# Kernel optimization log

Hardware: AMD Instinct MI355X
Metric: run time of the kernel (lower is better)

The kernel has to match this reference:

```python
import jax, jax.numpy as jnp
import numpy as np
import math

D_MODEL = 1024
N_HEADS = 16
D_HEAD = D_MODEL // N_HEADS
B, T = 2, 2048


def setup_inputs() -> dict:
    key = jax.random.key(0)
    ks = jax.random.split(key, 5)
    x = jax.random.normal(ks[0], (B, T, D_MODEL), dtype=jnp.float32)
    W_qkv = jax.random.normal(ks[1], (D_MODEL, 3 * D_MODEL), dtype=jnp.float32) * 0.02
    b_qkv = jnp.zeros((3 * D_MODEL,), dtype=jnp.float32)
    W_g = jax.random.normal(ks[2], (N_HEADS, D_HEAD, D_HEAD), dtype=jnp.float32) * 0.02
    W_out = jax.random.normal(ks[3], (D_MODEL, D_MODEL), dtype=jnp.float32) * 0.02
    b_out = jnp.zeros((D_MODEL,), dtype=jnp.float32)
    return {"x": x, "W_qkv": W_qkv, "b_qkv": b_qkv, "W_g": W_g, "W_out": W_out, "b_out": b_out}


def reference(x, W_qkv, b_qkv, W_g, W_out, b_out):
    b, t, d = x.shape
    h, dh = N_HEADS, D_HEAD
    qkv = x @ W_qkv + b_qkv                         # (B,T,3D)
    q, k, v = jnp.split(qkv, 3, axis=-1)
    # (B,T,D) -> (B,H,T,dh)
    q = q.reshape(b, t, h, dh).transpose(0, 2, 1, 3)
    k = k.reshape(b, t, h, dh).transpose(0, 2, 1, 3)
    v = v.reshape(b, t, h, dh).transpose(0, 2, 1, 3)
    scale = 1.0 / math.sqrt(dh)
    scores = jnp.einsum('bhtd,bhsd->bhts', q, k) * scale   # (B,H,T,T)
    causal = jnp.tril(jnp.ones((t, t), dtype=bool))
    scores = jnp.where(causal, scores, jnp.float32(-jnp.inf))
    attn = jax.nn.softmax(scores, axis=-1)
    # query-conditioned bilinear value gate (applied at each position)
    g = jax.nn.sigmoid(jnp.einsum('bhtd,hde->bhte', q, W_g))  # (B,H,T,dh)
    v = g * v
    out = jnp.einsum('bhts,bhsd->bhtd', attn, v)             # (B,H,T,dh)
    out = out.transpose(0, 2, 1, 3).reshape(b, t, d)
    return out @ W_out + b_out
```

## Files before the change

kernel.cpp:

```cpp
#include <hip/hip_runtime.h>
#include <hip/hip_bf16.h>

typedef unsigned short ushortT;
typedef __bf16 bf16x8 __attribute__((ext_vector_type(8)));
typedef float f32x4 __attribute__((ext_vector_type(4)));

#define T_SEQ 2048
#define DH 64
#define NH 16
#define DM 1024
#define TD 3072
#define BATCH 2
#define LOG2E 1.44269504f

#define BARRIER()   asm volatile("s_barrier" ::: "memory")
#define VMCNT(n)    asm volatile("s_waitcnt vmcnt(" #n ")" ::: "memory")

__device__ inline ushortT f2bf(float f){
    union { float f; unsigned int u; } a; a.f = f;
    unsigned int r = a.u + 0x7fffu + ((a.u >> 16) & 1u);
    return (ushortT)(r >> 16);
}
__device__ inline float bf2f(ushortT u){
    union { float f; unsigned int u; } a; a.u = ((unsigned int)u) << 16;
    return a.f;
}

__device__ inline void gload_lds16(const void* g, void* l){
    __builtin_amdgcn_global_load_lds((const __attribute__((address_space(1))) void*)g,
                                     (__attribute__((address_space(3))) void*)l, 16, 0, 0);
}

__global__ __launch_bounds__(256) void prep_kernel(const float* __restrict__ x,
                                                   ushortT* __restrict__ xbf,
                                                   const float* __restrict__ Wqkv,
                                                   ushortT* __restrict__ wqkvT,
                                                   const float* __restrict__ Wout,
                                                   ushortT* __restrict__ woutT,
                                                   const float* __restrict__ Wg,
                                                   ushortT* __restrict__ wgT){
    __shared__ float tile[64][65];
    int blk = blockIdx.x, tid = threadIdx.x;
    if (blk < 4096){
        int i = (blk * 256 + tid) * 4;
        float4 v = *(const float4*)&x[i];
        xbf[i+0] = f2bf(v.x); xbf[i+1] = f2bf(v.y);
        xbf[i+2] = f2bf(v.z); xbf[i+3] = f2bf(v.w);
        return;
    }
    int c = tid & 63, r4 = tid >> 6;
    if (blk >= 5120){
        int h = blk - 5120;
#pragma unroll
        for (int i = 0; i < 16; i++){
            int d = r4 + i*4;
            tile[d][c] = Wg[h*4096 + d*64 + c];
        }
        __syncthreads();
#pragma unroll
        for (int i = 0; i < 16; i++){
            int e = r4 + i*4;
            wgT[h*4096 + e*64 + c] = f2bf(tile[c][e]);
        }
        return;
    }
    const float* in; ushortT* out; int K, N, n0, k0;
    if (blk < 4864){
        int t = blk - 4096; in = Wqkv; out = wqkvT; K = 1024; N = 3072;
        n0 = (t % 48) * 64; k0 = (t / 48) * 64;
    } else {
        int t = blk - 4864; in = Wout; out = woutT; K = 1024; N = 1024;
        n0 = (t & 15) * 64; k0 = (t >> 4) * 64;
    }
#pragma unroll
    for (int i = 0; i < 16; i++){
        int k = r4 + i * 4;
        tile[k][c] = in[(size_t)(k0 + k) * N + n0 + c];
    }
    __syncthreads();
#pragma unroll
    for (int i = 0; i < 16; i++){
        int n = r4 + i * 4;
        out[(size_t)(n0 + n) * K + k0 + c] = f2bf(tile[c][n]);
    }
}

__global__ __launch_bounds__(256) void gemm_bf16_kernel(const ushortT* __restrict__ A,
                                                        const ushortT* __restrict__ BT,
                                                        const float* __restrict__ bias,
                                                        ushortT* __restrict__ C,
                                                        int M, int N, int K){
    __shared__ __align__(16) ushortT As[2][128*32];
    __shared__ __align__(16) ushortT Bs[2][128*32];
    int tid = threadIdx.x;
    int m0 = blockIdx.x * 128;
    int n0 = blockIdx.y * 128;
    int wid = tid >> 6, lane = tid & 63;
    int l15 = lane & 15, g = lane >> 4;
    int wr = wid >> 1, wc = wid & 1;

    f32x4 acc[4][4];
#pragma unroll
    for (int i = 0; i < 4; i++)
#pragma unroll
        for (int j = 0; j < 4; j++) acc[i][j] = (f32x4){0.f,0.f,0.f,0.f};

    int srow = wid * 32 + (lane >> 2);
    int sch  = lane & 3;

#define GSTAGE(buf, k0)                                                                  \
    {                                                                                    \
        _Pragma("unroll")                                                                \
        for (int i_ = 0; i_ < 2; i_++){                                                  \
            int row_ = srow + i_ * 16;                                                   \
            const ushortT* asrc_ = A  + (size_t)(m0 + row_) * K + (k0) + sch * 8;        \
            const ushortT* bsrc_ = BT + (size_t)(n0 + row_) * K + (k0) + sch * 8;        \
            gload_lds16(asrc_, (char*)As[buf] + (wid*2 + i_) * 1024);                    \
            gload_lds16(bsrc_, (char*)Bs[buf] + (wid*2 + i_) * 1024);                    \
        }                                                                                \
    }

    GSTAGE(0, 0);

    int nk = K >> 5;
    for (int kt = 0; kt < nk; kt++){
        int buf = kt & 1;
        BARRIER();
        if (kt + 1 < nk){
            GSTAGE(buf ^ 1, (kt + 1) * 32);
            VMCNT(4);
        } else {
            VMCNT(0);
        }
        BARRIER();

        bf16x8 af[4], bfr[4];
#pragma unroll
        for (int mi = 0; mi < 4; mi++){
            int r = wr*64 + mi*16 + l15;
            af[mi]  = *(const bf16x8*)(As[buf] + r*32 + g*8);
        }
#pragma unroll
        for (int ni = 0; ni < 4; ni++){
            int r = wc*64 + ni*16 + l15;
            bfr[ni] = *(const bf16x8*)(Bs[buf] + r*32 + g*8);
        }
#pragma unroll
        for (int mi = 0; mi < 4; mi++)
#pragma unroll
            for (int ni = 0; ni < 4; ni++)
                acc[mi][ni] = __builtin_amdgcn_mfma_f32_16x16x32_bf16(af[mi], bfr[ni], acc[mi][ni], 0, 0, 0);
    }
#undef GSTAGE

#pragma unroll
    for (int mi = 0; mi < 4; mi++){
#pragma unroll
        for (int jj = 0; jj < 4; jj++){
            int mm = m0 + wr*64 + mi*16 + 4*g + jj;
#pragma unroll
            for (int ni = 0; ni < 4; ni++){
                int nn = n0 + wc*64 + ni*16 + l15;
                C[(size_t)mm * N + nn] = f2bf(acc[mi][ni][jj] + bias[nn]);
            }
        }
    }
}

__global__ __launch_bounds__(256) void gemm_out_kernel(const ushortT* __restrict__ A,
                                                       const ushortT* __restrict__ BT,
                                                       const float* __restrict__ bias,
                                                       float* __restrict__ C,
                                                       int M, int N, int K){
    __shared__ __align__(16) ushortT As[2][64*32];
    __shared__ __align__(16) ushortT Bs[2][128*32];
    int tid = threadIdx.x;
    int m0 = blockIdx.x * 64;
    int n0 = blockIdx.y * 128;
    int wid = tid >> 6, lane = tid & 63;
    int l15 = lane & 15, g = lane >> 4;
    int wr = wid >> 1, wc = wid & 1;

    f32x4 acc[2][4];
#pragma unroll
    for (int i = 0; i < 2; i++)
#pragma unroll
        for (int j = 0; j < 4; j++) acc[i][j] = (f32x4){0.f,0.f,0.f,0.f};

    int srow = tid >> 2;
    int sch  = tid & 3;

#define GSTAGE(buf, k0)                                                                  \
    {                                                                                    \
        gload_lds16(A + (size_t)(m0 + srow) * K + (k0) + sch * 8,                        \
                    (char*)As[buf] + tid * 16);                                          \
        _Pragma("unroll")                                                                \
        for (int i_ = 0; i_ < 2; i_++){                                                  \
            int row_ = srow + i_ * 64;                                                   \
            gload_lds16(BT + (size_t)(n0 + row_) * K + (k0) + sch * 8,                   \
                        (char*)Bs[buf] + (i_*256 + tid) * 16);                           \
        }                                                                                \
    }

    GSTAGE(0, 0);

    int nk = K >> 5;
    for (int kt = 0; kt < nk; kt++){
        int buf = kt & 1;
        BARRIER();
        if (kt + 1 < nk){
            GSTAGE(buf ^ 1, (kt + 1) * 32);
            VMCNT(3);
        } else {
            VMCNT(0);
        }
        BARRIER();

        bf16x8 af[2], bfr[4];
#pragma unroll
        for (int mi = 0; mi < 2; mi++){
            int r = wr*32 + mi*16 + l15;
            af[mi]  = *(const bf16x8*)(As[buf] + r*32 + g*8);
        }
#pragma unroll
        for (int ni = 0; ni < 4; ni++){
            int r = wc*64 + ni*16 + l15;
            bfr[ni] = *(const bf16x8*)(Bs[buf] + r*32 + g*8);
        }
#pragma unroll
        for (int mi = 0; mi < 2; mi++)
#pragma unroll
            for (int ni = 0; ni < 4; ni++)
                acc[mi][ni] = __builtin_amdgcn_mfma_f32_16x16x32_bf16(af[mi], bfr[ni], acc[mi][ni], 0, 0, 0);
    }
#undef GSTAGE

#pragma unroll
    for (int mi = 0; mi < 2; mi++){
#pragma unroll
        for (int jj = 0; jj < 4; jj++){
            int mm = m0 + wr*32 + mi*16 + 4*g + jj;
#pragma unroll
            for (int ni = 0; ni < 4; ni++){
                int nn = n0 + wc*64 + ni*16 + l15;
                C[(size_t)mm * N + nn] = acc[mi][ni][jj] + bias[nn];
            }
        }
    }
}

__global__ __launch_bounds__(256) void gate_kernel(const ushortT* __restrict__ qkv,
                                                   const ushortT* __restrict__ WgT,
                                                   ushortT* __restrict__ vgT){
    __shared__ __align__(16) ushortT VT[64][72];
    int tblk = blockIdx.x, bh = blockIdx.y;
    int b = bh >> 4, h = bh & 15;
    int tid = threadIdx.x, wid = tid >> 6, lane = tid & 63;
    int l15 = lane & 15, g = lane >> 4;
    int t0 = tblk * 64;
    int tl = wid*16 + l15;

    const ushortT* qrow = qkv + ((size_t)b*T_SEQ + t0 + tl)*TD + h*DH;
    bf16x8 qf0 = *(const bf16x8*)(qrow + 8*g);
    bf16x8 qf1 = *(const bf16x8*)(qrow + 32 + 8*g);

    const ushortT* wbase = WgT + h*4096;
    const ushortT* vrow = qkv + ((size_t)b*T_SEQ + t0 + tl)*TD + 2*DM + h*DH;

#pragma unroll
    for (int ns = 0; ns < 4; ns++){
        int e = ns*16 + l15;
        bf16x8 wf0 = *(const bf16x8*)(wbase + e*64 + 8*g);
        bf16x8 wf1 = *(const bf16x8*)(wbase + e*64 + 32 + 8*g);
        f32x4 z = (f32x4){0.f,0.f,0.f,0.f};
        z = __builtin_amdgcn_mfma_f32_16x16x32_bf16(wf0, qf0, z, 0, 0, 0);
        z = __builtin_amdgcn_mfma_f32_16x16x32_bf16(wf1, qf1, z, 0, 0, 0);
        union { ushortT u[4]; uint2 v; } v4;
        v4.v = *(const uint2*)(vrow + ns*16 + 4*g);
#pragma unroll
        for (int jj = 0; jj < 4; jj++){
            float ex = __builtin_amdgcn_exp2f(-z[jj] * LOG2E);
            float gv = __builtin_amdgcn_rcpf(1.f + ex);
            VT[ns*16 + 4*g + jj][tl] = f2bf(gv * bf2f(v4.u[jj]));
        }
    }
    __syncthreads();
    for (int i = tid; i < 64*8; i += 256){
        int e = i >> 3, c8 = (i & 7) * 8;
        *(uint4*)&vgT[((size_t)bh * DH + e) * T_SEQ + t0 + c8] = *(const uint4*)&VT[e][c8];
    }
}

struct QS {
    bf16x8 qf0, qf1;
    float m_, lsum;
    f32x4 acc[4];
};

__device__ __forceinline__ void proc2(const ushortT* __restrict__ K0,
                                      const ushortT* __restrict__ V0,
                                      const ushortT* __restrict__ K1,
                                      const ushortT* __restrict__ V1,
                                      QS& S, int t0, int t1, int myp,
                                      int wq, int l15, int g){
    int l7 = l15 & 7;
    f32x4 s[8];
    __builtin_amdgcn_s_setprio(1);
#pragma unroll
    for (int ns = 0; ns < 4; ns++){
        int kr = ns*16 + l15;
        bf16x8 kf0 = *(const bf16x8*)(K0 + kr*64 + ((g    ) ^ l7)*8);
        bf16x8 kf1 = *(const bf16x8*)(K0 + kr*64 + ((4 + g) ^ l7)*8);
        f32x4 z = (f32x4){0.f,0.f,0.f,0.f};
        z = __builtin_amdgcn_mfma_f32_16x16x32_bf16(kf0, S.qf0, z, 0, 0, 0);
        z = __builtin_amdgcn_mfma_f32_16x16x32_bf16(kf1, S.qf1, z, 0, 0, 0);
        s[ns] = z;
    }
#pragma unroll
    for (int ns = 0; ns < 4; ns++){
        int kr = ns*16 + l15;
        bf16x8 kf0 = *(const bf16x8*)(K1 + kr*64 + ((g    ) ^ l7)*8);
        bf16x8 kf1 = *(const bf16x8*)(K1 + kr*64 + ((4 + g) ^ l7)*8);
        f32x4 z = (f32x4){0.f,0.f,0.f,0.f};
        z = __builtin_amdgcn_mfma_f32_16x16x32_bf16(kf0, S.qf0, z, 0, 0, 0);
        z = __builtin_amdgcn_mfma_f32_16x16x32_bf16(kf1, S.qf1, z, 0, 0, 0);
        s[4 + ns] = z;
    }
    __builtin_amdgcn_s_setprio(0);

    int qrel = wq*16 + l15;
    bool diag0 = (t0 == myp);
    bool inv1  = (t1 > myp);
    bool diag1 = (t1 == myp);
    if (diag0){
#pragma unroll
        for (int ns = 0; ns < 4; ns++){
            int kb = ((ns & 2) << 4) + 8*g + ((ns & 1) << 2);
#pragma unroll
            for (int jj = 0; jj < 4; jj++)
                if (kb + jj > qrel) s[ns][jj] = -INFINITY;
        }
    }
    if (inv1){
#pragma unroll
        for (int ns = 0; ns < 4; ns++)
#pragma unroll
            for (int jj = 0; jj < 4; jj++) s[4+ns][jj] = -INFINITY;
    } else if (diag1){
#pragma unroll
        for (int ns = 0; ns < 4; ns++){
            int kb = ((ns & 2) << 4) + 8*g + ((ns & 1) << 2);
#pragma unroll
            for (int jj = 0; jj < 4; jj++)
                if (kb + jj > qrel) s[4+ns][jj] = -INFINITY;
        }
    }

    float tmax = -INFINITY;
#pragma unroll
    for (int ns = 0; ns < 8; ns++){
        float a = fmaxf(s[ns][0], s[ns][1]);
        float c = fmaxf(s[ns][2], s[ns][3]);
        tmax = fmaxf(tmax, fmaxf(a, c));
    }
    tmax = fmaxf(tmax, __shfl_xor(tmax, 16, 64));
    tmax = fmaxf(tmax, __shfl_xor(tmax, 32, 64));

    float mnew = fmaxf(S.m_, tmax);
    float mc = mnew * LOG2E;
    float rs = 0.f;
    bf16x8 pa[4];
#pragma unroll
    for (int pr = 0; pr < 4; pr++){
#pragma unroll
        for (int jj = 0; jj < 4; jj++){
            float p0 = __builtin_amdgcn_exp2f(fmaf(s[2*pr  ][jj], LOG2E, -mc));
            float p1 = __builtin_amdgcn_exp2f(fmaf(s[2*pr+1][jj], LOG2E, -mc));
            rs += p0 + p1;
            pa[pr][jj]   = (__bf16)p0;
            pa[pr][4+jj] = (__bf16)p1;
        }
    }
    rs += __shfl_xor(rs, 16, 64);
    rs += __shfl_xor(rs, 32, 64);

    if (!__all(mnew == S.m_)){
        float alpha = __builtin_amdgcn_exp2f(fmaf(S.m_, LOG2E, -mc));
#pragma unroll
        for (int nt = 0; nt < 4; nt++)
#pragma unroll
            for (int jj = 0; jj < 4; jj++) S.acc[nt][jj] *= alpha;
        S.lsum *= alpha;
        S.m_ = mnew;
    }
    S.lsum += rs;

    __builtin_amdgcn_s_setprio(1);
#pragma unroll
    for (int ks = 0; ks < 2; ks++){
#pragma unroll
        for (int nt = 0; nt < 4; nt++){
            bf16x8 vf = *(const bf16x8*)(V0 + (nt*16 + l15)*64 + ((ks*4 + g) ^ l7)*8);
            S.acc[nt] = __builtin_amdgcn_mfma_f32_16x16x32_bf16(vf, pa[ks], S.acc[nt], 0, 0, 0);
        }
    }
    if (!inv1){
#pragma unroll
        for (int ks = 0; ks < 2; ks++){
#pragma unroll
            for (int nt = 0; nt < 4; nt++){
                bf16x8 vf = *(const bf16x8*)(V1 + (nt*16 + l15)*64 + ((ks*4 + g) ^ l7)*8);
                S.acc[nt] = __builtin_amdgcn_mfma_f32_16x16x32_bf16(vf, pa[2+ks], S.acc[nt], 0, 0, 0);
            }
        }
    }
    __builtin_amdgcn_s_setprio(0);
}

__global__ __launch_bounds__(512, 2) void attn_kernel(const ushortT* __restrict__ qkv,
                                                      const ushortT* __restrict__ vgT,
                                                      ushortT* __restrict__ obf){
    __shared__ __align__(16) ushortT Ks[2][2][64*64];
    __shared__ __align__(16) ushortT Vs[2][2][64*64];
    int bh = blockIdx.x, y = blockIdx.y;
    int pairid = (y < 8) ? y : 23 - y;
    int b = bh >> 4, h = bh & 15;
    int tid = threadIdx.x, wid = tid >> 6, lane = tid & 63;
    int l15 = lane & 15, g = lane >> 4;
    int grp = wid >> 2;
    int wq  = wid & 3;

    const ushortT* Kg = qkv + (size_t)b * T_SEQ * TD + DM + h * DH;
    const ushortT* Vg = vgT + (size_t)bh * DH * T_SEQ;

    int pA = pairid, pB = 31 - pairid;
    int myp = grp ? pB : pA;

    int st_row  = tid >> 3;
    int st_c    = (tid & 7) ^ (st_row & 7);
    int st_prow = (st_row & 0x20) | ((st_row & 0x0C) << 1) |
                  ((st_row & 0x10) >> 2) | (st_row & 3);

#define STAGE_ROUND(buf, rr)                                                             \
    {                                                                                    \
        int t0_ = 2*(rr);     if (t0_ > pB) t0_ = pB;                                    \
        int t1_ = 2*(rr) + 1; if (t1_ > pB) t1_ = pB;                                    \
        gload_lds16(Kg + (size_t)(t0_*64 + st_prow) * TD + st_c*8,                       \
                    (char*)Ks[buf][0] + tid*16);                                         \
        gload_lds16(Kg + (size_t)(t1_*64 + st_prow) * TD + st_c*8,                       \
                    (char*)Ks[buf][1] + tid*16);                                         \
        gload_lds16(Vg + (size_t)st_row * T_SEQ + t0_*64 + st_c*8,                       \
                    (char*)Vs[buf][0] + tid*16);                                         \
        gload_lds16(Vg + (size_t)st_row * T_SEQ + t1_*64 + st_c*8,                       \
                    (char*)Vs[buf][1] + tid*16);                                         \
    }

    QS S;
    {
        int qrow = myp*64 + wq*16 + l15;
        const ushortT* qb = qkv + ((size_t)b * T_SEQ + qrow) * TD + h * DH;
        S.qf0 = *(const bf16x8*)(qb + 8*g);
        S.qf1 = *(const bf16x8*)(qb + 32 + 8*g);
#pragma unroll
        for (int j = 0; j < 8; j++){
            S.qf0[j] = (__bf16)((float)S.qf0[j] * 0.125f);
            S.qf1[j] = (__bf16)((float)S.qf1[j] * 0.125f);
        }
        S.m_ = -INFINITY; S.lsum = 0.f;
#pragma unroll
        for (int nt = 0; nt < 4; nt++) S.acc[nt] = (f32x4){0.f,0.f,0.f,0.f};
    }

    int nr = (33 - pairid) >> 1;
    STAGE_ROUND(0, 0);

    for (int r = 0; r < nr; r++){
        int buf = r & 1;
        BARRIER();
        if (r + 1 < nr){
            STAGE_ROUND(buf ^ 1, r + 1);
            VMCNT(4);
        } else {
            VMCNT(0);
        }
        BARRIER();
        int t0 = 2*r;
        if (t0 <= myp)
            proc2(Ks[buf][0], Vs[buf][0], Ks[buf][1], Vs[buf][1],
                  S, t0, t0 + 1, myp, wq, l15, g);
    }
#undef STAGE_ROUND

    float inv = 1.f / S.lsum;
    size_t orow = ((size_t)b * T_SEQ + myp*64 + wq*16 + l15) * DM + h*DH;
#pragma unroll
    for (int nt = 0; nt < 4; nt++){
        union { ushortT u[4]; uint2 v; } pk;
#pragma unroll
        for (int jj = 0; jj < 4; jj++) pk.u[jj] = f2bf(S.acc[nt][jj] * inv);
        *(uint2*)&obf[orow + nt*16 + 4*g] = pk.v;
    }
}

extern "C" void kernel_launch(void* const* d_in, const int* in_sizes, int n_in,
                              void* d_out, int out_size, void* d_ws, size_t ws_size,
                              hipStream_t stream){
    const float* x    = (const float*)d_in[0];
    const float* Wqkv = (const float*)d_in[1];
    const float* bqkv = (const float*)d_in[2];
    const float* Wg   = (const float*)d_in[3];
    const float* Wout = (const float*)d_in[4];
    const float* bout = (const float*)d_in[5];

    char* ws = (char*)d_ws;
    ushortT* xbf   = (ushortT*)(ws);
    ushortT* wqkvT = (ushortT*)(ws + 8388608);
    ushortT* woutT = (ushortT*)(ws + 14680064);
    ushortT* qkvb  = (ushortT*)(ws + 16777216);
    ushortT* vgT   = (ushortT*)(ws + 41943040);
    ushortT* obf   = (ushortT*)(ws + 50331648);
    ushortT* wgT   = (ushortT*)(ws + 58720256);

    prep_kernel<<<5136, 256, 0, stream>>>(x, xbf, Wqkv, wqkvT, Wout, woutT, Wg, wgT);
    gemm_bf16_kernel<<<dim3(32,24), 256, 0, stream>>>(xbf, wqkvT, bqkv, qkvb, 4096, 3072, 1024);
    gate_kernel<<<dim3(32,32), 256, 0, stream>>>(qkvb, wgT, vgT);
    attn_kernel<<<dim3(32,16), 512, 0, stream>>>(qkvb, vgT, obf);
    gemm_out_kernel<<<dim3(64,8), 256, 0, stream>>>(obf, woutT, bout, (float*)d_out, 4096, 1024, 1024);
}
```

Baseline: 110.1 us.

## Switch attention to 32x32x16 MFMA with 32-row query tiles per wave

```diff
diff --git a/kernel.cpp b/kernel.cpp
--- a/kernel.cpp
+++ b/kernel.cpp
@@ -4,6 +4,7 @@
 typedef unsigned short ushortT;
 typedef __bf16 bf16x8 __attribute__((ext_vector_type(8)));
 typedef float f32x4 __attribute__((ext_vector_type(4)));
+typedef float f32x16 __attribute__((ext_vector_type(16)));
 
 #define T_SEQ 2048
 #define DH 64
@@ -291,133 +292,117 @@
     }
 }
 
-struct QS {
-    bf16x8 qf0, qf1;
+struct QS32 {
+    bf16x8 qf[4];
     float m_, lsum;
-    f32x4 acc[4];
+    f32x16 acc[2];
 };
 
-__device__ __forceinline__ void proc2(const ushortT* __restrict__ K0,
-                                      const ushortT* __restrict__ V0,
-                                      const ushortT* __restrict__ K1,
-                                      const ushortT* __restrict__ V1,
-                                      QS& S, int t0, int t1, int myp,
-                                      int wq, int l15, int g){
-    int l7 = l15 & 7;
-    f32x4 s[8];
-    __builtin_amdgcn_s_setprio(1);
-#pragma unroll
-    for (int ns = 0; ns < 4; ns++){
-        int kr = ns*16 + l15;
-        bf16x8 kf0 = *(const bf16x8*)(K0 + kr*64 + ((g    ) ^ l7)*8);
-        bf16x8 kf1 = *(const bf16x8*)(K0 + kr*64 + ((4 + g) ^ l7)*8);
-        f32x4 z = (f32x4){0.f,0.f,0.f,0.f};
-        z = __builtin_amdgcn_mfma_f32_16x16x32_bf16(kf0, S.qf0, z, 0, 0, 0);
-        z = __builtin_amdgcn_mfma_f32_16x16x32_bf16(kf1, S.qf1, z, 0, 0, 0);
-        s[ns] = z;
-    }
-#pragma unroll
-    for (int ns = 0; ns < 4; ns++){
-        int kr = ns*16 + l15;
-        bf16x8 kf0 = *(const bf16x8*)(K1 + kr*64 + ((g    ) ^ l7)*8);
-        bf16x8 kf1 = *(const bf16x8*)(K1 + kr*64 + ((4 + g) ^ l7)*8);
-        f32x4 z = (f32x4){0.f,0.f,0.f,0.f};
-        z = __builtin_amdgcn_mfma_f32_16x16x32_bf16(kf0, S.qf0, z, 0, 0, 0);
-        z = __builtin_amdgcn_mfma_f32_16x16x32_bf16(kf1, S.qf1, z, 0, 0, 0);
-        s[4 + ns] = z;
-    }
-    __builtin_amdgcn_s_setprio(0);
-
-    int qrel = wq*16 + l15;
+__device__ __forceinline__ void proc32(const ushortT* __restrict__ K0,
+                                       const ushortT* __restrict__ V0,
+                                       const ushortT* __restrict__ K1,
+                                       const ushortT* __restrict__ V1,
+                                       QS32& S, int t0, int t1, int myp,
+                                       int qrel, int q32, int hi){
+    int x7 = q32 & 7;
     bool diag0 = (t0 == myp);
     bool inv1  = (t1 > myp);
     bool diag1 = (t1 == myp);
+
+    f32x16 s[2][2];
+    __builtin_amdgcn_s_setprio(1);
+#pragma unroll
+    for (int T = 0; T < 2; T++){
+        if (T == 1 && inv1) break;
+        const ushortT* Kb = T ? K1 : K0;
+#pragma unroll
+        for (int h2 = 0; h2 < 2; h2++){
+            f32x16 z;
+#pragma unroll
+            for (int i = 0; i < 16; i++) z[i] = 0.f;
+#pragma unroll
+            for (int c = 0; c < 4; c++){
+                bf16x8 kf = *(const bf16x8*)(Kb + (32*h2 + q32)*64 + (((2*c + hi) ^ x7) * 8));
+                z = __builtin_amdgcn_mfma_f32_32x32x16_bf16(kf, S.qf[c], z, 0, 0, 0);
+            }
+            s[T][h2] = z;
+        }
+    }
+    __builtin_amdgcn_s_setprio(0);
+
     if (diag0){
 #pragma unroll
-        for (int ns = 0; ns < 4; ns++){
-            int kb = ((ns & 2) << 4) + 8*g + ((ns & 1) << 2);
-#pragma unroll
-            for (int jj = 0; jj < 4; jj++)
-                if (kb + jj > qrel) s[ns][jj] = -INFINITY;
-        }
-    }
-    if (inv1){
-#pragma unroll
-        for (int ns = 0; ns < 4; ns++)
-#pragma unroll
-            for (int jj = 0; jj < 4; jj++) s[4+ns][jj] = -INFINITY;
-    } else if (diag1){
-#pragma unroll
-        for (int ns = 0; ns < 4; ns++){
-            int kb = ((ns & 2) << 4) + 8*g + ((ns & 1) << 2);
-#pragma unroll
-            for (int jj = 0; jj < 4; jj++)
-                if (kb + jj > qrel) s[4+ns][jj] = -INFINITY;
-        }
+        for (int h2 = 0; h2 < 2; h2++)
+#pragma unroll
+            for (int r = 0; r < 16; r++){
+                int klog = 32*h2 + 16*(r>>3) + 4*((r>>2)&1) + (r&3);
+                if (klog + 8*hi > qrel) s[0][h2][r] = -INFINITY;
+            }
+    }
+    if (!inv1 && diag1){
+#pragma unroll
+        for (int h2 = 0; h2 < 2; h2++)
+#pragma unroll
+            for (int r = 0; r < 16; r++){
+                int klog = 32*h2 + 16*(r>>3) + 4*((r>>2)&1) + (r&3);
+                if (klog + 8*hi > qrel) s[1][h2][r] = -INFINITY;
+            }
     }
 
     float tmax = -INFINITY;
 #pragma unroll
-    for (int ns = 0; ns < 8; ns++){
-        float a = fmaxf(s[ns][0], s[ns][1]);
-        float c = fmaxf(s[ns][2], s[ns][3]);
-        tmax = fmaxf(tmax, fmaxf(a, c));
-    }
-    tmax = fmaxf(tmax, __shfl_xor(tmax, 16, 64));
+    for (int T = 0; T < 2; T++){
+        if (T == 1 && inv1) break;
+#pragma unroll
+        for (int h2 = 0; h2 < 2; h2++)
+#pragma unroll
+            for (int r = 0; r < 16; r++) tmax = fmaxf(tmax, s[T][h2][r]);
+    }
     tmax = fmaxf(tmax, __shfl_xor(tmax, 32, 64));
 
     float mnew = fmaxf(S.m_, tmax);
     float mc = mnew * LOG2E;
-    float rs = 0.f;
-    bf16x8 pa[4];
-#pragma unroll
-    for (int pr = 0; pr < 4; pr++){
-#pragma unroll
-        for (int jj = 0; jj < 4; jj++){
-            float p0 = __builtin_amdgcn_exp2f(fmaf(s[2*pr  ][jj], LOG2E, -mc));
-            float p1 = __builtin_amdgcn_exp2f(fmaf(s[2*pr+1][jj], LOG2E, -mc));
-            rs += p0 + p1;
-            pa[pr][jj]   = (__bf16)p0;
-            pa[pr][4+jj] = (__bf16)p1;
-        }
-    }
-    rs += __shfl_xor(rs, 16, 64);
-    rs += __shfl_xor(rs, 32, 64);
-
     if (!__all(mnew == S.m_)){
         float alpha = __builtin_amdgcn_exp2f(fmaf(S.m_, LOG2E, -mc));
 #pragma unroll
-        for (int nt = 0; nt < 4; nt++)
-#pragma unroll
-            for (int jj = 0; jj < 4; jj++) S.acc[nt][jj] *= alpha;
+        for (int eh = 0; eh < 2; eh++)
+#pragma unroll
+            for (int i = 0; i < 16; i++) S.acc[eh][i] *= alpha;
         S.lsum *= alpha;
         S.m_ = mnew;
     }
+
+    float rs = 0.f;
+    __builtin_amdgcn_s_setprio(1);
+#pragma unroll
+    for (int T = 0; T < 2; T++){
+        if (T == 1 && inv1) break;
+        const ushortT* Vb = T ? V1 : V0;
+#pragma unroll
+        for (int ck = 0; ck < 4; ck++){
+            bf16x8 pa;
+            int h2 = ck >> 1;
+#pragma unroll
+            for (int j = 0; j < 8; j++){
+                int r = 8*(ck & 1) + 4*(j >> 2) + (j & 3);
+                float p = __builtin_amdgcn_exp2f(fmaf(s[T][h2][r], LOG2E, -mc));
+                rs += p;
+                pa[j] = (__bf16)p;
+            }
+#pragma unroll
+            for (int eh = 0; eh < 2; eh++){
+                bf16x8 vf = *(const bf16x8*)(Vb + (32*eh + q32)*64 + (((2*ck + hi) ^ x7) * 8));
+                S.acc[eh] = __builtin_amdgcn_mfma_f32_32x32x16_bf16(vf, pa, S.acc[eh], 0, 0, 0);
+            }
+        }
+    }
+    __builtin_amdgcn_s_setprio(0);
+
+    rs += __shfl_xor(rs, 32, 64);
     S.lsum += rs;
-
-    __builtin_amdgcn_s_setprio(1);
-#pragma unroll
-    for (int ks = 0; ks < 2; ks++){
-#pragma unroll
-        for (int nt = 0; nt < 4; nt++){
-            bf16x8 vf = *(const bf16x8*)(V0 + (nt*16 + l15)*64 + ((ks*4 + g) ^ l7)*8);
-            S.acc[nt] = __builtin_amdgcn_mfma_f32_16x16x32_bf16(vf, pa[ks], S.acc[nt], 0, 0, 0);
-        }
-    }
-    if (!inv1){
-#pragma unroll
-        for (int ks = 0; ks < 2; ks++){
-#pragma unroll
-            for (int nt = 0; nt < 4; nt++){
-                bf16x8 vf = *(const bf16x8*)(V1 + (nt*16 + l15)*64 + ((ks*4 + g) ^ l7)*8);
-                S.acc[nt] = __builtin_amdgcn_mfma_f32_16x16x32_bf16(vf, pa[2+ks], S.acc[nt], 0, 0, 0);
-            }
-        }
-    }
-    __builtin_amdgcn_s_setprio(0);
-}
-
-__global__ __launch_bounds__(512, 2) void attn_kernel(const ushortT* __restrict__ qkv,
+}
+
+__global__ __launch_bounds__(256, 2) void attn_kernel(const ushortT* __restrict__ qkv,
                                                       const ushortT* __restrict__ vgT,
                                                       ushortT* __restrict__ obf){
     __shared__ __align__(16) ushortT Ks[2][2][64*64];
@@ -426,49 +411,57 @@
     int pairid = (y < 8) ? y : 23 - y;
     int b = bh >> 4, h = bh & 15;
     int tid = threadIdx.x, wid = tid >> 6, lane = tid & 63;
-    int l15 = lane & 15, g = lane >> 4;
-    int grp = wid >> 2;
-    int wq  = wid & 3;
+    int q32 = lane & 31, hi = lane >> 5;
+    int grp = wid >> 1;
+    int qh  = wid & 1;
 
     const ushortT* Kg = qkv + (size_t)b * T_SEQ * TD + DM + h * DH;
     const ushortT* Vg = vgT + (size_t)bh * DH * T_SEQ;
 
     int pA = pairid, pB = 31 - pairid;
     int myp = grp ? pB : pA;
-
-    int st_row  = tid >> 3;
-    int st_c    = (tid & 7) ^ (st_row & 7);
-    int st_prow = (st_row & 0x20) | ((st_row & 0x0C) << 1) |
-                  ((st_row & 0x10) >> 2) | (st_row & 3);
+    int qrel = qh*32 + q32;
+
+    int sr  = tid >> 3;
+    int sc8 = tid & 7;
 
 #define STAGE_ROUND(buf, rr)                                                             \
     {                                                                                    \
         int t0_ = 2*(rr);     if (t0_ > pB) t0_ = pB;                                    \
         int t1_ = 2*(rr) + 1; if (t1_ > pB) t1_ = pB;                                    \
-        gload_lds16(Kg + (size_t)(t0_*64 + st_prow) * TD + st_c*8,                       \
-                    (char*)Ks[buf][0] + tid*16);                                         \
-        gload_lds16(Kg + (size_t)(t1_*64 + st_prow) * TD + st_c*8,                       \
-                    (char*)Ks[buf][1] + tid*16);                                         \
-        gload_lds16(Vg + (size_t)st_row * T_SEQ + t0_*64 + st_c*8,                       \
-                    (char*)Vs[buf][0] + tid*16);                                         \
-        gload_lds16(Vg + (size_t)st_row * T_SEQ + t1_*64 + st_c*8,                       \
-                    (char*)Vs[buf][1] + tid*16);                                         \
-    }
-
-    QS S;
+        _Pragma("unroll")                                                                \
+        for (int i_ = 0; i_ < 2; i_++){                                                  \
+            int row_ = sr + 32*i_;                                                       \
+            int sc_  = sc8 ^ (row_ & 7);                                                 \
+            int r32_ = row_ & 31;                                                        \
+            int pr_  = 32*i_ + ((r32_ & ~12) | ((r32_ & 4) << 1) | ((r32_ & 8) >> 1));   \
+            gload_lds16(Kg + (size_t)(t0_*64 + pr_) * TD + sc_*8,                        \
+                        (char*)Ks[buf][0] + tid*16 + i_*4096);                           \
+            gload_lds16(Kg + (size_t)(t1_*64 + pr_) * TD + sc_*8,                        \
+                        (char*)Ks[buf][1] + tid*16 + i_*4096);                           \
+            gload_lds16(Vg + (size_t)row_ * T_SEQ + t0_*64 + sc_*8,                      \
+                        (char*)Vs[buf][0] + tid*16 + i_*4096);                           \
+            gload_lds16(Vg + (size_t)row_ * T_SEQ + t1_*64 + sc_*8,                      \
+                        (char*)Vs[buf][1] + tid*16 + i_*4096);                           \
+        }                                                                                \
+    }
+
+    QS32 S;
     {
-        int qrow = myp*64 + wq*16 + l15;
-        const ushortT* qb = qkv + ((size_t)b * T_SEQ + qrow) * TD + h * DH;
-        S.qf0 = *(const bf16x8*)(qb + 8*g);
-        S.qf1 = *(const bf16x8*)(qb + 32 + 8*g);
-#pragma unroll
-        for (int j = 0; j < 8; j++){
-            S.qf0[j] = (__bf16)((float)S.qf0[j] * 0.125f);
-            S.qf1[j] = (__bf16)((float)S.qf1[j] * 0.125f);
+        int qrow = myp*64 + qrel;
+        const ushortT* qb = qkv + ((size_t)b * T_SEQ + qrow) * TD + h * DH + 8*hi;
+#pragma unroll
+        for (int c = 0; c < 4; c++){
+            S.qf[c] = *(const bf16x8*)(qb + 16*c);
+#pragma unroll
+            for (int j = 0; j < 8; j++)
+                S.qf[c][j] = (__bf16)((float)S.qf[c][j] * 0.125f);
         }
         S.m_ = -INFINITY; S.lsum = 0.f;
 #pragma unroll
-        for (int nt = 0; nt < 4; nt++) S.acc[nt] = (f32x4){0.f,0.f,0.f,0.f};
+        for (int eh = 0; eh < 2; eh++)
+#pragma unroll
+            for (int i = 0; i < 16; i++) S.acc[eh][i] = 0.f;
     }
 
     int nr = (33 - pairid) >> 1;
@@ -479,26 +472,30 @@
         BARRIER();
         if (r + 1 < nr){
             STAGE_ROUND(buf ^ 1, r + 1);
-            VMCNT(4);
+            VMCNT(8);
         } else {
             VMCNT(0);
         }
         BARRIER();
         int t0 = 2*r;
         if (t0 <= myp)
-            proc2(Ks[buf][0], Vs[buf][0], Ks[buf][1], Vs[buf][1],
-                  S, t0, t0 + 1, myp, wq, l15, g);
+            proc32(Ks[buf][0], Vs[buf][0], Ks[buf][1], Vs[buf][1],
+                   S, t0, t0 + 1, myp, qrel, q32, hi);
     }
 #undef STAGE_ROUND
 
     float inv = 1.f / S.lsum;
-    size_t orow = ((size_t)b * T_SEQ + myp*64 + wq*16 + l15) * DM + h*DH;
-#pragma unroll
-    for (int nt = 0; nt < 4; nt++){
-        union { ushortT u[4]; uint2 v; } pk;
-#pragma unroll
-        for (int jj = 0; jj < 4; jj++) pk.u[jj] = f2bf(S.acc[nt][jj] * inv);
-        *(uint2*)&obf[orow + nt*16 + 4*g] = pk.v;
+    size_t orow = ((size_t)b * T_SEQ + myp*64 + qrel) * DM + h*DH;
+#pragma unroll
+    for (int eh = 0; eh < 2; eh++){
+#pragma unroll
+        for (int a = 0; a < 4; a++){
+            union { ushortT u[4]; uint2 v; } pk;
+#pragma unroll
+            for (int bb = 0; bb < 4; bb++)
+                pk.u[bb] = f2bf(S.acc[eh][4*a + bb] * inv);
+            *(uint2*)&obf[orow + 32*eh + 8*a + 4*hi] = pk.v;
+        }
     }
 }
 
@@ -524,6 +521,6 @@
     prep_kernel<<<5136, 256, 0, stream>>>(x, xbf, Wqkv, wqkvT, Wout, woutT, Wg, wgT);
     gemm_bf16_kernel<<<dim3(32,24), 256, 0, stream>>>(xbf, wqkvT, bqkv, qkvb, 4096, 3072, 1024);
     gate_kernel<<<dim3(32,32), 256, 0, stream>>>(qkvb, wgT, vgT);
-    attn_kernel<<<dim3(32,16), 512, 0, stream>>>(qkvb, vgT, obf);
+    attn_kernel<<<dim3(32,16), 256, 0, stream>>>(qkvb, vgT, obf);
     gemm_out_kernel<<<dim3(64,8), 256, 0, stream>>>(obf, woutT, bout, (float*)d_out, 4096, 1024, 1024);
 }
```

Result: slower. 114.1 us (+3.7%).
